# Kernel tuning notes

Hardware: AMD Instinct MI355X
Metric: run time of the kernel (lower is better)

## Reference

```python
import jax, jax.numpy as jnp
import numpy as np

D_MODEL = 1024
N_HEADS = 8
D_KEYS = D_MODEL // N_HEADS  # 128
D_LLM = 4096


def setup_inputs() -> dict:
    key = jax.random.key(0)
    ks = jax.random.split(key, 11)
    Bm, Lq, Vs = 8, 1024, 2048
    inner = D_KEYS * N_HEADS  # 1024
    s = 0.02
    return {
        "Q": jax.random.normal(ks[0], (Bm, Lq, D_MODEL), jnp.float32),
        "K_src": jax.random.normal(ks[1], (Vs, D_LLM), jnp.float32),
        "V_src": jax.random.normal(ks[2], (Vs, D_LLM), jnp.float32),
        "Wq": jax.random.normal(ks[3], (D_MODEL, inner), jnp.float32) * s,
        "bq": jnp.zeros((inner,), jnp.float32),
        "Wk": jax.random.normal(ks[4], (D_LLM, inner), jnp.float32) * s,
        "bk": jnp.zeros((inner,), jnp.float32),
        "Wv": jax.random.normal(ks[5], (D_LLM, inner), jnp.float32) * s,
        "bv": jnp.zeros((inner,), jnp.float32),
        "Wo": jax.random.normal(ks[6], (inner, D_LLM), jnp.float32) * s,
        "bo": jnp.zeros((D_LLM,), jnp.float32),
    }


def reference(Q, K_src, V_src, Wq, bq, Wk, bk, Wv, bv, Wo, bo):
    Bm, Lq, _ = Q.shape
    Vs, d_llm = K_src.shape
    H = N_HEADS
    Ek = d_llm // H  # NOTE: torch code scales by d_llm//H, not d_keys
    q = (Q @ Wq + bq).reshape(Bm, Lq, H, -1)           # [B,Lq,H,E]
    k = (K_src @ Wk + bk).reshape(Vs, H, -1)            # [S,H,E]
    v = (V_src @ Wv + bv).reshape(Vs, H, -1)            # [S,H,E]
    scale = 1.0 / jnp.sqrt(jnp.asarray(Ek, q.dtype))
    scores = jnp.einsum("blhe,she->bhls", q, k)         # [B,H,Lq,S]
    A = jax.nn.softmax(scale * scores, axis=-1)         # dropout = identity (eval)
    out = jnp.einsum("bhls,she->blhe", A, v)            # [B,Lq,H,E]
    out = out.reshape(Bm, Lq, -1)
    return out @ Wo + bo                                 # [B,Lq,d_llm]
```

## Files before the change

### kernel.cpp

```cpp
#include <hip/hip_runtime.h>
#include <hip/hip_bf16.h>


typedef __bf16 bf16x8 __attribute__((ext_vector_type(8)));
typedef float  f32x4  __attribute__((ext_vector_type(4)));

union V16 { uint4 u; bf16x8 v; };
__device__ __forceinline__ bf16x8 ld16v(const void* p) {
  V16 t; t.u = *(const uint4*)p; return t.v;
}
__device__ __forceinline__ uint4 pack8(float4 a, float4 b) {
  V16 t;
  t.v[0] = (__bf16)a.x; t.v[1] = (__bf16)a.y; t.v[2] = (__bf16)a.z; t.v[3] = (__bf16)a.w;
  t.v[4] = (__bf16)b.x; t.v[5] = (__bf16)b.y; t.v[6] = (__bf16)b.z; t.v[7] = (__bf16)b.w;
  return t.u;
}
__device__ __forceinline__ void dma16(const void* g, void* l) {
  __builtin_amdgcn_global_load_lds(
      (const __attribute__((address_space(1))) unsigned int*)g,
      (__attribute__((address_space(3))) unsigned int*)l, 16, 0, 0);
}
__device__ __forceinline__ int chunk_of(int row, int gc) {
  return row * 4 + (gc ^ ((row >> 1) & 3));
}

__global__ __launch_bounds__(256) void transpose_k(const float* __restrict__ W,
                                                   __bf16* __restrict__ Wt, int K, int N) {
  __shared__ __bf16 t[32][33];
  int tx = threadIdx.x & 31, ty = threadIdx.x >> 5;
  int n0 = blockIdx.x * 32, k0 = blockIdx.y * 32;
#pragma unroll
  for (int r = 0; r < 32; r += 8) t[ty + r][tx] = (__bf16)W[(size_t)(k0 + ty + r) * N + n0 + tx];
  __syncthreads();
#pragma unroll
  for (int r = 0; r < 32; r += 8) Wt[(size_t)(n0 + ty + r) * K + k0 + tx] = t[tx][ty + r];
}

template <typename AT, typename CT>
__device__ __forceinline__ void gemm_core(__bf16* As, __bf16* Bs,
                                          const AT* __restrict__ A,
                                          const __bf16* __restrict__ Bt,
                                          const float* __restrict__ bias,
                                          CT* __restrict__ C,
                                          int M, int N, int K, int lda, int trans,
                                          int m0, int n0) {
  const int tid = threadIdx.x;
  const int lane = tid & 63, wave = tid >> 6;
  const int g = lane >> 4, l16 = lane & 15;
  const int wr = wave >> 1, wc = wave & 1;
  int aoff[4], boff[4];
#pragma unroll
  for (int mf = 0; mf < 4; mf++) aoff[mf] = chunk_of(wr * 64 + mf * 16 + l16, g) * 8;
#pragma unroll
  for (int nf = 0; nf < 4; nf++) boff[nf] = chunk_of(wc * 64 + nf * 16 + l16, g) * 8;

  f32x4 acc[4][4] = {};
  for (int k0 = 0; k0 < K; k0 += 32) {
    __syncthreads();
    if constexpr (sizeof(AT) == 2) {
#pragma unroll
      for (int rnd = 0; rnd < 2; rnd++) {
        int cstart = wave * 128 + rnd * 64;
        int p = cstart + lane;
        int row = p >> 2, gc = (p & 3) ^ ((row >> 1) & 3);
        dma16((const __bf16*)A + (size_t)(m0 + row) * lda + k0 + gc * 8,
              As + (size_t)cstart * 8);
      }
    } else {
#pragma unroll
      for (int i = 0; i < 2; i++) {
        int p = tid + i * 256;
        int row = p >> 2, gc = (p & 3) ^ ((row >> 1) & 3);
        const float* ap = (const float*)A + (size_t)(m0 + row) * lda + k0 + gc * 8;
        float4 f0 = *(const float4*)ap;
        float4 f1 = *(const float4*)(ap + 4);
        *(uint4*)(As + p * 8) = pack8(f0, f1);
      }
    }
#pragma unroll
    for (int rnd = 0; rnd < 2; rnd++) {
      int cstart = wave * 128 + rnd * 64;
      int p = cstart + lane;
      int row = p >> 2, gc = (p & 3) ^ ((row >> 1) & 3);
      dma16(Bt + (size_t)(n0 + row) * (size_t)K + k0 + gc * 8,
            Bs + (size_t)cstart * 8);
    }
    __syncthreads();
    bf16x8 af[4], bff[4];
#pragma unroll
    for (int mf = 0; mf < 4; mf++) af[mf]  = ld16v(As + aoff[mf]);
#pragma unroll
    for (int nf = 0; nf < 4; nf++) bff[nf] = ld16v(Bs + boff[nf]);
#pragma unroll
    for (int mf = 0; mf < 4; mf++)
#pragma unroll
      for (int nf = 0; nf < 4; nf++)
        acc[mf][nf] = __builtin_amdgcn_mfma_f32_16x16x32_bf16(af[mf], bff[nf], acc[mf][nf], 0, 0, 0);
  }
#pragma unroll
  for (int nf = 0; nf < 4; nf++) {
    int col = n0 + wc * 64 + nf * 16 + l16;
    float bv = bias[col];
#pragma unroll
    for (int mf = 0; mf < 4; mf++) {
      int rowb = m0 + wr * 64 + mf * 16 + g * 4;
      if constexpr (sizeof(CT) == 2) {
        if (trans) {
          union { __bf16 h[4]; uint2 u; } pk;
#pragma unroll
          for (int r = 0; r < 4; r++) pk.h[r] = (__bf16)(acc[mf][nf][r] + bv);
          *(uint2*)&((__bf16*)C)[(size_t)col * M + rowb] = pk.u;
        } else {
#pragma unroll
          for (int r = 0; r < 4; r++)
            ((__bf16*)C)[(size_t)(rowb + r) * N + col] = (__bf16)(acc[mf][nf][r] + bv);
        }
      } else {
#pragma unroll
        for (int r = 0; r < 4; r++)
          ((float*)C)[(size_t)(rowb + r) * N + col] = acc[mf][nf][r] + bv;
      }
    }
  }
}

__global__ __launch_bounds__(256) void gemm_f_b(const float* __restrict__ A,
                                                const __bf16* __restrict__ Bt,
                                                const float* __restrict__ bias,
                                                __bf16* __restrict__ C,
                                                int M, int N, int K, int lda, int trans) {
  __shared__ __align__(16) __bf16 As[128 * 32];
  __shared__ __align__(16) __bf16 Bs[128 * 32];
  gemm_core<float, __bf16>(As, Bs, A, Bt, bias, C, M, N, K, lda, trans,
                           blockIdx.x * 128, blockIdx.y * 128);
}

__global__ __launch_bounds__(256) void gemm_b_f(const __bf16* __restrict__ A,
                                                const __bf16* __restrict__ Bt,
                                                const float* __restrict__ bias,
                                                float* __restrict__ C,
                                                int M, int N, int K, int lda, int trans) {
  __shared__ __align__(16) __bf16 As[128 * 32];
  __shared__ __align__(16) __bf16 Bs[128 * 32];
  gemm_core<__bf16, float>(As, Bs, A, Bt, bias, C, M, N, K, lda, trans,
                           blockIdx.x * 128, blockIdx.y * 128);
}

__global__ __launch_bounds__(256) void gemm_kv(const float* __restrict__ A0, const __bf16* __restrict__ B0t,
                                               const float* __restrict__ b0, __bf16* __restrict__ C0,
                                               const float* __restrict__ A1, const __bf16* __restrict__ B1t,
                                               const float* __restrict__ b1, __bf16* __restrict__ C1) {
  __shared__ __align__(16) __bf16 As[128 * 32];
  __shared__ __align__(16) __bf16 Bs[128 * 32];
  if (blockIdx.z == 0)
    gemm_core<float, __bf16>(As, Bs, A0, B0t, b0, C0, 2048, 1024, 4096, 4096, 0,
                             blockIdx.x * 128, blockIdx.y * 128);
  else
    gemm_core<float, __bf16>(As, Bs, A1, B1t, b1, C1, 2048, 1024, 4096, 4096, 1,
                             blockIdx.x * 128, blockIdx.y * 128);
}

__global__ __launch_bounds__(256) void attn_k(const __bf16* __restrict__ q,
                                              const __bf16* __restrict__ k,
                                              const __bf16* __restrict__ vt,
                                              __bf16* __restrict__ o) {
  __shared__ union {
    __bf16 ks[64][136];
    __bf16 ps[128][72];
  } u;
  __shared__ __bf16 vs[128][72];
  const int tid = threadIdx.x, lane = tid & 63, wave = tid >> 6;
  const int g = lane >> 4, l16 = lane & 15;
  const int h = blockIdx.y, q0 = blockIdx.x * 128;
  const float scale = 0.044194173824159216f;

  bf16x8 qf[2][4];
#pragma unroll
  for (int mf = 0; mf < 2; mf++)
#pragma unroll
    for (int kk = 0; kk < 4; kk++) {
      int row = q0 + wave * 32 + mf * 16 + l16;
      qf[mf][kk] = ld16v(q + (size_t)row * 1024 + h * 128 + kk * 32 + g * 8);
    }

  f32x4 accO[2][8] = {};
  float m_i[2][4], l_i[2][4];
#pragma unroll
  for (int a = 0; a < 2; a++)
#pragma unroll
    for (int b = 0; b < 4; b++) { m_i[a][b] = -1e30f; l_i[a][b] = 0.f; }

  for (int s0 = 0; s0 < 2048; s0 += 64) {
    __syncthreads();
#pragma unroll
    for (int i = 0; i < 4; i++) {
      int c = tid + i * 256;
      { int row = c >> 4, col = (c & 15) * 8;
        *(uint4*)&u.ks[row][col] = *(const uint4*)(k + (size_t)(s0 + row) * 1024 + h * 128 + col); }
      { int row = c >> 3, col = (c & 7) * 8;
        *(uint4*)&vs[row][col] = *(const uint4*)(vt + (size_t)(h * 128 + row) * 2048 + s0 + col); }
    }
    __syncthreads();

    f32x4 sc[2][4] = {};
#pragma unroll
    for (int kk = 0; kk < 4; kk++) {
      bf16x8 kf[4];
#pragma unroll
      for (int nf = 0; nf < 4; nf++) kf[nf] = ld16v(&u.ks[nf * 16 + l16][kk * 32 + g * 8]);
#pragma unroll
      for (int mf = 0; mf < 2; mf++)
#pragma unroll
        for (int nf = 0; nf < 4; nf++)
          sc[mf][nf] = __builtin_amdgcn_mfma_f32_16x16x32_bf16(qf[mf][kk], kf[nf], sc[mf][nf], 0, 0, 0);
    }
#pragma unroll
    for (int mf = 0; mf < 2; mf++)
#pragma unroll
      for (int nf = 0; nf < 4; nf++) sc[mf][nf] *= scale;

#pragma unroll
    for (int mf = 0; mf < 2; mf++)
#pragma unroll
      for (int r = 0; r < 4; r++) {
        float mx = fmaxf(fmaxf(sc[mf][0][r], sc[mf][1][r]), fmaxf(sc[mf][2][r], sc[mf][3][r]));
#pragma unroll
        for (int off = 1; off < 16; off <<= 1) mx = fmaxf(mx, __shfl_xor(mx, off));
        float mo = m_i[mf][r];
        float mn = fmaxf(mo, mx);
        float alpha = __expf(mo - mn);
        float rs = 0.f;
#pragma unroll
        for (int nf = 0; nf < 4; nf++) {
          float p = __expf(sc[mf][nf][r] - mn);
          sc[mf][nf][r] = p;
          rs += p;
        }
#pragma unroll
        for (int off = 1; off < 16; off <<= 1) rs += __shfl_xor(rs, off);
        m_i[mf][r] = mn;
        l_i[mf][r] = l_i[mf][r] * alpha + rs;
#pragma unroll
        for (int ef = 0; ef < 8; ef++) accO[mf][ef][r] *= alpha;
      }

    __syncthreads();

#pragma unroll
    for (int mf = 0; mf < 2; mf++)
#pragma unroll
      for (int r = 0; r < 4; r++) {
        int prow = wave * 32 + mf * 16 + g * 4 + r;
#pragma unroll
        for (int nf = 0; nf < 4; nf++) u.ps[prow][nf * 16 + l16] = (__bf16)sc[mf][nf][r];
      }

#pragma unroll
    for (int kk = 0; kk < 2; kk++) {
      bf16x8 pf[2];
#pragma unroll
      for (int mf = 0; mf < 2; mf++) pf[mf] = ld16v(&u.ps[wave * 32 + mf * 16 + l16][kk * 32 + g * 8]);
#pragma unroll
      for (int ef = 0; ef < 8; ef++) {
        bf16x8 vf = ld16v(&vs[ef * 16 + l16][kk * 32 + g * 8]);
#pragma unroll
        for (int mf = 0; mf < 2; mf++)
          accO[mf][ef] = __builtin_amdgcn_mfma_f32_16x16x32_bf16(pf[mf], vf, accO[mf][ef], 0, 0, 0);
      }
    }
  }

#pragma unroll
  for (int mf = 0; mf < 2; mf++)
#pragma unroll
    for (int ef = 0; ef < 8; ef++)
#pragma unroll
      for (int r = 0; r < 4; r++) {
        int row = q0 + wave * 32 + mf * 16 + g * 4 + r;
        int col = h * 128 + ef * 16 + l16;
        o[(size_t)row * 1024 + col] = (__bf16)(accO[mf][ef][r] / l_i[mf][r]);
      }
}

extern "C" void kernel_launch(void* const* d_in, const int* in_sizes, int n_in,
                              void* d_out, int out_size, void* d_ws, size_t ws_size,
                              hipStream_t stream) {
  const float* Q   = (const float*)d_in[0];
  const float* Ksr = (const float*)d_in[1];
  const float* Vsr = (const float*)d_in[2];
  const float* Wq  = (const float*)d_in[3];
  const float* bq  = (const float*)d_in[4];
  const float* Wk  = (const float*)d_in[5];
  const float* bk  = (const float*)d_in[6];
  const float* Wv  = (const float*)d_in[7];
  const float* bv  = (const float*)d_in[8];
  const float* Wo  = (const float*)d_in[9];
  const float* bo  = (const float*)d_in[10];
  __bf16* ws = (__bf16*)d_ws;
  const size_t MB = 1024 * 1024;
  __bf16* qb  = ws;
  __bf16* kb  = ws + 8  * MB;
  __bf16* vtb = ws + 10 * MB;
  __bf16* at  = ws + 12 * MB;
  __bf16* WqT = ws + 20 * MB;
  __bf16* WkT = ws + 21 * MB;
  __bf16* WvT = ws + 25 * MB;
  __bf16* WoT = ws + 29 * MB;

  transpose_k<<<dim3(32, 32),  256, 0, stream>>>(Wq, WqT, 1024, 1024);
  transpose_k<<<dim3(32, 128), 256, 0, stream>>>(Wk, WkT, 4096, 1024);
  transpose_k<<<dim3(32, 128), 256, 0, stream>>>(Wv, WvT, 4096, 1024);
  transpose_k<<<dim3(128, 32), 256, 0, stream>>>(Wo, WoT, 1024, 4096);

  gemm_f_b<<<dim3(64, 8), 256, 0, stream>>>(Q, WqT, bq, qb, 8192, 1024, 1024, 1024, 0);
  gemm_kv<<<dim3(16, 8, 2), 256, 0, stream>>>(Ksr, WkT, bk, kb, Vsr, WvT, bv, vtb);
  attn_k<<<dim3(64, 8), 256, 0, stream>>>(qb, kb, vtb, at);
  gemm_b_f<<<dim3(64, 32), 256, 0, stream>>>(at, WoT, bo, (float*)d_out, 8192, 4096, 1024, 1024, 0);
}
```

Before: 720.3 us.

## Retile attention to 64-row blocks, fold softmax scale into Wq, DMA swizzled K/V loads

The attention kernel now handles 64 query rows per block instead of 128, which doubles the grid to 1024 blocks and raises the occupancy hint to 4 blocks per CU. The softmax scale and log2(e) are folded into the Wq weights and the bq bias, so the kernel can call exp2f directly and skip the per-tile multiply. K and V tiles are loaded with direct global-to-LDS DMA into an XOR-swizzled layout to avoid bank conflicts, and MFMA phases are wrapped in setprio. In exchange, each K/V tile is now reused across fewer query rows, so global and L2 traffic for K/V goes up.

```diff
diff --git a/kernel.cpp b/kernel.cpp
--- a/kernel.cpp
+++ b/kernel.cpp
@@ -25,12 +25,14 @@
 }
 
 __global__ __launch_bounds__(256) void transpose_k(const float* __restrict__ W,
-                                                   __bf16* __restrict__ Wt, int K, int N) {
+                                                   __bf16* __restrict__ Wt, int K, int N,
+                                                   float scale) {
   __shared__ __bf16 t[32][33];
   int tx = threadIdx.x & 31, ty = threadIdx.x >> 5;
   int n0 = blockIdx.x * 32, k0 = blockIdx.y * 32;
 #pragma unroll
-  for (int r = 0; r < 32; r += 8) t[ty + r][tx] = (__bf16)W[(size_t)(k0 + ty + r) * N + n0 + tx];
+  for (int r = 0; r < 32; r += 8)
+    t[ty + r][tx] = (__bf16)(W[(size_t)(k0 + ty + r) * N + n0 + tx] * scale);
   __syncthreads();
 #pragma unroll
   for (int r = 0; r < 32; r += 8) Wt[(size_t)(n0 + ty + r) * K + k0 + tx] = t[tx][ty + r];
@@ -43,7 +45,7 @@
                                           const float* __restrict__ bias,
                                           CT* __restrict__ C,
                                           int M, int N, int K, int lda, int trans,
-                                          int m0, int n0) {
+                                          int m0, int n0, float bscale) {
   const int tid = threadIdx.x;
   const int lane = tid & 63, wave = tid >> 6;
   const int g = lane >> 4, l16 = lane & 15;
@@ -100,7 +102,7 @@
 #pragma unroll
   for (int nf = 0; nf < 4; nf++) {
     int col = n0 + wc * 64 + nf * 16 + l16;
-    float bv = bias[col];
+    float bv = bias[col] * bscale;
 #pragma unroll
     for (int mf = 0; mf < 4; mf++) {
       int rowb = m0 + wr * 64 + mf * 16 + g * 4;
@@ -128,11 +130,12 @@
                                                 const __bf16* __restrict__ Bt,
                                                 const float* __restrict__ bias,
                                                 __bf16* __restrict__ C,
-                                                int M, int N, int K, int lda, int trans) {
+                                                int M, int N, int K, int lda, int trans,
+                                                float bscale) {
   __shared__ __align__(16) __bf16 As[128 * 32];
   __shared__ __align__(16) __bf16 Bs[128 * 32];
   gemm_core<float, __bf16>(As, Bs, A, Bt, bias, C, M, N, K, lda, trans,
-                           blockIdx.x * 128, blockIdx.y * 128);
+                           blockIdx.x * 128, blockIdx.y * 128, bscale);
 }
 
 __global__ __launch_bounds__(256) void gemm_b_f(const __bf16* __restrict__ A,
@@ -143,7 +146,7 @@
   __shared__ __align__(16) __bf16 As[128 * 32];
   __shared__ __align__(16) __bf16 Bs[128 * 32];
   gemm_core<__bf16, float>(As, Bs, A, Bt, bias, C, M, N, K, lda, trans,
-                           blockIdx.x * 128, blockIdx.y * 128);
+                           blockIdx.x * 128, blockIdx.y * 128, 1.0f);
 }
 
 __global__ __launch_bounds__(256) void gemm_kv(const float* __restrict__ A0, const __bf16* __restrict__ B0t,
@@ -154,132 +157,125 @@
   __shared__ __align__(16) __bf16 Bs[128 * 32];
   if (blockIdx.z == 0)
     gemm_core<float, __bf16>(As, Bs, A0, B0t, b0, C0, 2048, 1024, 4096, 4096, 0,
-                             blockIdx.x * 128, blockIdx.y * 128);
+                             blockIdx.x * 128, blockIdx.y * 128, 1.0f);
   else
     gemm_core<float, __bf16>(As, Bs, A1, B1t, b1, C1, 2048, 1024, 4096, 4096, 1,
-                             blockIdx.x * 128, blockIdx.y * 128);
-}
-
-__global__ __launch_bounds__(256) void attn_k(const __bf16* __restrict__ q,
-                                              const __bf16* __restrict__ k,
-                                              const __bf16* __restrict__ vt,
-                                              __bf16* __restrict__ o) {
-  __shared__ union {
-    __bf16 ks[64][136];
-    __bf16 ps[128][72];
+                             blockIdx.x * 128, blockIdx.y * 128, 1.0f);
+}
+
+__global__ __launch_bounds__(256, 4) void attn_k(const __bf16* __restrict__ q,
+                                                 const __bf16* __restrict__ k,
+                                                 const __bf16* __restrict__ vt,
+                                                 __bf16* __restrict__ o) {
+  __shared__ __align__(16) union {
+    __bf16 ks[64 * 128];
+    __bf16 ps[64 * 72];
   } u;
-  __shared__ __bf16 vs[128][72];
+  __shared__ __align__(16) __bf16 vs[128 * 64];
   const int tid = threadIdx.x, lane = tid & 63, wave = tid >> 6;
   const int g = lane >> 4, l16 = lane & 15;
-  const int h = blockIdx.y, q0 = blockIdx.x * 128;
-  const float scale = 0.044194173824159216f;
-
-  bf16x8 qf[2][4];
-#pragma unroll
-  for (int mf = 0; mf < 2; mf++)
-#pragma unroll
-    for (int kk = 0; kk < 4; kk++) {
-      int row = q0 + wave * 32 + mf * 16 + l16;
-      qf[mf][kk] = ld16v(q + (size_t)row * 1024 + h * 128 + kk * 32 + g * 8);
-    }
-
-  f32x4 accO[2][8] = {};
-  float m_i[2][4], l_i[2][4];
-#pragma unroll
-  for (int a = 0; a < 2; a++)
-#pragma unroll
-    for (int b = 0; b < 4; b++) { m_i[a][b] = -1e30f; l_i[a][b] = 0.f; }
+  const int h = blockIdx.y, q0 = blockIdx.x * 64;
+
+  bf16x8 qf[4];
+#pragma unroll
+  for (int kk = 0; kk < 4; kk++)
+    qf[kk] = ld16v(q + (size_t)(q0 + wave * 16 + l16) * 1024 + h * 128 + kk * 32 + g * 8);
+
+  f32x4 accO[8] = {};
+  float m_i[4], l_i[4];
+#pragma unroll
+  for (int r = 0; r < 4; r++) { m_i[r] = -1e30f; l_i[r] = 0.f; }
 
   for (int s0 = 0; s0 < 2048; s0 += 64) {
     __syncthreads();
 #pragma unroll
     for (int i = 0; i < 4; i++) {
-      int c = tid + i * 256;
-      { int row = c >> 4, col = (c & 15) * 8;
-        *(uint4*)&u.ks[row][col] = *(const uint4*)(k + (size_t)(s0 + row) * 1024 + h * 128 + col); }
-      { int row = c >> 3, col = (c & 7) * 8;
-        *(uint4*)&vs[row][col] = *(const uint4*)(vt + (size_t)(h * 128 + row) * 2048 + s0 + col); }
-    }
-    __syncthreads();
-
-    f32x4 sc[2][4] = {};
+      int c = wave * 256 + i * 64 + lane;
+      int row = c >> 4, gc = (c & 15) ^ (row & 7);
+      dma16(k + (size_t)(s0 + row) * 1024 + h * 128 + gc * 8,
+            u.ks + (wave * 256 + i * 64) * 8);
+    }
+#pragma unroll
+    for (int i = 0; i < 4; i++) {
+      int c = wave * 256 + i * 64 + lane;
+      int row = c >> 3, cc = (c & 7) ^ (row & 7);
+      dma16(vt + (size_t)(h * 128 + row) * 2048 + s0 + cc * 8,
+            vs + (wave * 256 + i * 64) * 8);
+    }
+    __syncthreads();
+
+    f32x4 sc[4] = {};
+    __builtin_amdgcn_s_setprio(1);
 #pragma unroll
     for (int kk = 0; kk < 4; kk++) {
       bf16x8 kf[4];
 #pragma unroll
-      for (int nf = 0; nf < 4; nf++) kf[nf] = ld16v(&u.ks[nf * 16 + l16][kk * 32 + g * 8]);
-#pragma unroll
-      for (int mf = 0; mf < 2; mf++)
-#pragma unroll
-        for (int nf = 0; nf < 4; nf++)
-          sc[mf][nf] = __builtin_amdgcn_mfma_f32_16x16x32_bf16(qf[mf][kk], kf[nf], sc[mf][nf], 0, 0, 0);
-    }
-#pragma unroll
-    for (int mf = 0; mf < 2; mf++)
-#pragma unroll
-      for (int nf = 0; nf < 4; nf++) sc[mf][nf] *= scale;
-
-#pragma unroll
-    for (int mf = 0; mf < 2; mf++)
+      for (int nf = 0; nf < 4; nf++) {
+        int row = nf * 16 + l16;
+        kf[nf] = ld16v(u.ks + (row * 16 + ((kk * 4 + g) ^ (row & 7))) * 8);
+      }
+#pragma unroll
+      for (int nf = 0; nf < 4; nf++)
+        sc[nf] = __builtin_amdgcn_mfma_f32_16x16x32_bf16(qf[kk], kf[nf], sc[nf], 0, 0, 0);
+    }
+    __builtin_amdgcn_s_setprio(0);
+
+#pragma unroll
+    for (int r = 0; r < 4; r++) {
+      float mx = fmaxf(fmaxf(sc[0][r], sc[1][r]), fmaxf(sc[2][r], sc[3][r]));
+#pragma unroll
+      for (int off = 1; off < 16; off <<= 1) mx = fmaxf(mx, __shfl_xor(mx, off));
+      float mn = fmaxf(m_i[r], mx);
+      float alpha = exp2f(m_i[r] - mn);
+      float rs = 0.f;
+#pragma unroll
+      for (int nf = 0; nf < 4; nf++) {
+        float p = exp2f(sc[nf][r] - mn);
+        sc[nf][r] = p;
+        rs += p;
+      }
+#pragma unroll
+      for (int off = 1; off < 16; off <<= 1) rs += __shfl_xor(rs, off);
+      m_i[r] = mn;
+      l_i[r] = l_i[r] * alpha + rs;
+#pragma unroll
+      for (int ef = 0; ef < 8; ef++) accO[ef][r] *= alpha;
+    }
+
+    __syncthreads();
+
+#pragma unroll
+    for (int nf = 0; nf < 4; nf++)
 #pragma unroll
       for (int r = 0; r < 4; r++) {
-        float mx = fmaxf(fmaxf(sc[mf][0][r], sc[mf][1][r]), fmaxf(sc[mf][2][r], sc[mf][3][r]));
-#pragma unroll
-        for (int off = 1; off < 16; off <<= 1) mx = fmaxf(mx, __shfl_xor(mx, off));
-        float mo = m_i[mf][r];
-        float mn = fmaxf(mo, mx);
-        float alpha = __expf(mo - mn);
-        float rs = 0.f;
-#pragma unroll
-        for (int nf = 0; nf < 4; nf++) {
-          float p = __expf(sc[mf][nf][r] - mn);
-          sc[mf][nf][r] = p;
-          rs += p;
-        }
-#pragma unroll
-        for (int off = 1; off < 16; off <<= 1) rs += __shfl_xor(rs, off);
-        m_i[mf][r] = mn;
-        l_i[mf][r] = l_i[mf][r] * alpha + rs;
-#pragma unroll
-        for (int ef = 0; ef < 8; ef++) accO[mf][ef][r] *= alpha;
-      }
-
-    __syncthreads();
-
-#pragma unroll
-    for (int mf = 0; mf < 2; mf++)
-#pragma unroll
-      for (int r = 0; r < 4; r++) {
-        int prow = wave * 32 + mf * 16 + g * 4 + r;
-#pragma unroll
-        for (int nf = 0; nf < 4; nf++) u.ps[prow][nf * 16 + l16] = (__bf16)sc[mf][nf][r];
-      }
-
+        int prow = wave * 16 + g * 4 + r;
+        u.ps[prow * 72 + nf * 16 + l16] = (__bf16)sc[nf][r];
+      }
+
+    __builtin_amdgcn_s_setprio(1);
 #pragma unroll
     for (int kk = 0; kk < 2; kk++) {
-      bf16x8 pf[2];
-#pragma unroll
-      for (int mf = 0; mf < 2; mf++) pf[mf] = ld16v(&u.ps[wave * 32 + mf * 16 + l16][kk * 32 + g * 8]);
+      bf16x8 pf = ld16v(u.ps + (wave * 16 + l16) * 72 + kk * 32 + g * 8);
 #pragma unroll
       for (int ef = 0; ef < 8; ef++) {
-        bf16x8 vf = ld16v(&vs[ef * 16 + l16][kk * 32 + g * 8]);
-#pragma unroll
-        for (int mf = 0; mf < 2; mf++)
-          accO[mf][ef] = __builtin_amdgcn_mfma_f32_16x16x32_bf16(pf[mf], vf, accO[mf][ef], 0, 0, 0);
-      }
-    }
+        int vrow = ef * 16 + l16;
+        bf16x8 vf = ld16v(vs + (vrow * 8 + ((kk * 4 + g) ^ (vrow & 7))) * 8);
+        accO[ef] = __builtin_amdgcn_mfma_f32_16x16x32_bf16(pf, vf, accO[ef], 0, 0, 0);
+      }
+    }
+    __builtin_amdgcn_s_setprio(0);
   }
 
-#pragma unroll
-  for (int mf = 0; mf < 2; mf++)
-#pragma unroll
-    for (int ef = 0; ef < 8; ef++)
-#pragma unroll
-      for (int r = 0; r < 4; r++) {
-        int row = q0 + wave * 32 + mf * 16 + g * 4 + r;
-        int col = h * 128 + ef * 16 + l16;
-        o[(size_t)row * 1024 + col] = (__bf16)(accO[mf][ef][r] / l_i[mf][r]);
-      }
+  float inv[4];
+#pragma unroll
+  for (int r = 0; r < 4; r++) inv[r] = 1.0f / l_i[r];
+#pragma unroll
+  for (int ef = 0; ef < 8; ef++)
+#pragma unroll
+    for (int r = 0; r < 4; r++) {
+      int row = q0 + wave * 16 + g * 4 + r;
+      o[(size_t)row * 1024 + h * 128 + ef * 16 + l16] = (__bf16)(accO[ef][r] * inv[r]);
+    }
 }
 
 extern "C" void kernel_launch(void* const* d_in, const int* in_sizes, int n_in,
@@ -307,13 +303,15 @@
   __bf16* WvT = ws + 25 * MB;
   __bf16* WoT = ws + 29 * MB;
 
-  transpose_k<<<dim3(32, 32),  256, 0, stream>>>(Wq, WqT, 1024, 1024);
-  transpose_k<<<dim3(32, 128), 256, 0, stream>>>(Wk, WkT, 4096, 1024);
-  transpose_k<<<dim3(32, 128), 256, 0, stream>>>(Wv, WvT, 4096, 1024);
-  transpose_k<<<dim3(128, 32), 256, 0, stream>>>(Wo, WoT, 1024, 4096);
-
-  gemm_f_b<<<dim3(64, 8), 256, 0, stream>>>(Q, WqT, bq, qb, 8192, 1024, 1024, 1024, 0);
+  const float qscale = 0.044194173824159216f * 1.4426950408889634f;
+
+  transpose_k<<<dim3(32, 32),  256, 0, stream>>>(Wq, WqT, 1024, 1024, qscale);
+  transpose_k<<<dim3(32, 128), 256, 0, stream>>>(Wk, WkT, 4096, 1024, 1.0f);
+  transpose_k<<<dim3(32, 128), 256, 0, stream>>>(Wv, WvT, 4096, 1024, 1.0f);
+  transpose_k<<<dim3(128, 32), 256, 0, stream>>>(Wo, WoT, 1024, 4096, 1.0f);
+
+  gemm_f_b<<<dim3(64, 8), 256, 0, stream>>>(Q, WqT, bq, qb, 8192, 1024, 1024, 1024, 0, qscale);
   gemm_kv<<<dim3(16, 8, 2), 256, 0, stream>>>(Ksr, WkT, bk, kb, Vsr, WvT, bv, vtb);
-  attn_k<<<dim3(64, 8), 256, 0, stream>>>(qb, kb, vtb, at);
+  attn_k<<<dim3(128, 8), 256, 0, stream>>>(qb, kb, vtb, at);
   gemm_b_f<<<dim3(64, 32), 256, 0, stream>>>(at, WoT, bo, (float*)d_out, 8192, 4096, 1024, 1024, 0);
 }
```

Result: faster. 682.9 us (-5.2%).
